# Kernel tuning notes

Measured on AMD Instinct MI355X. Metric: run time of the kernel, lower is better.

## Reference

```python
import jax, jax.numpy as jnp
import numpy as np

N, C, T, V, D = 128, 64, 256, 25, 64  # batch(*persons), in_ch, frames, joints, out_ch
RED = 4  # SE reduction


def _shift_indices(c, d, v):
    i = np.arange(v)[:, None]
    j = np.arange(c)[None, :]
    shift_in = ((i * c + j + j * c) % (c * v)).reshape(-1)
    jd = np.arange(d)[None, :]
    shift_out = ((i * d + jd - jd * d) % (d * v)).reshape(-1)
    return jnp.asarray(shift_in, jnp.int32), jnp.asarray(shift_out, jnp.int32)


def setup_inputs() -> dict:
    key = jax.random.key(0)
    ks = jax.random.split(key, 6)
    r = C // RED
    x0 = jax.random.normal(ks[0], (N, C, T, V), jnp.float32)
    fc1_w = jax.random.normal(ks[1], (r, C), jnp.float32) * (2.0 / C) ** 0.5
    fc1_b = jnp.zeros((r,), jnp.float32)
    fc2_w = jax.random.normal(ks[2], (4, r), jnp.float32) * (2.0 / r) ** 0.5
    fc2_b = jnp.zeros((4,), jnp.float32)
    W = jax.random.normal(ks[3], (4, C, D), jnp.float32) * (1.0 / D) ** 0.5
    b = jnp.zeros((4, D), jnp.float32)
    mask = jax.random.normal(ks[4], (1, V, C), jnp.float32) * 0.1  # Feature_Mask
    gamma = jnp.ones((V * D,), jnp.float32)
    beta = jnp.zeros((V * D,), jnp.float32)
    shift_in, shift_out = _shift_indices(C, D, V)
    return dict(x0=x0, epoch=100, fc1_w=fc1_w, fc1_b=fc1_b, fc2_w=fc2_w,
                fc2_b=fc2_b, W=W, b=b, mask=mask, gamma=gamma, beta=beta,
                shift_in=shift_in, shift_out=shift_out)


def reference(x0, epoch, fc1_w, fc1_b, fc2_w, fc2_b, W, b, mask, gamma, beta,
              shift_in, shift_out):
    n, c, t, v = x0.shape
    d = W.shape[-1]
    # DY_SEModule: global avg pool -> 1x1 conv -> relu -> 1x1 conv -> softmax(/tao)
    pooled = x0.mean(axis=(2, 3))                       # [n, c]
    h = jax.nn.relu(pooled @ fc1_w.T + fc1_b)           # [n, c//4]
    logits = h @ fc2_w.T + fc2_b                        # [n, 4]
    tao = 1.0 if epoch >= 60 else -(30.0 - 1.0) / 60.0 * epoch + 30.0
    gate = jax.nn.softmax(logits / tao, axis=1)         # [n, 4]
    # per-sample fused weights/bias
    Wf = jnp.einsum('kcd,nk->ncd', W, gate)             # [n, c, d]
    bf = jnp.einsum('kc,nk->nc', b, gate)               # [n, d]
    # shift-in gather + tanh feature mask
    x = x0.transpose(0, 2, 3, 1).reshape(n * t, v * c)  # [n*t, v*c]
    x = jnp.take(x, shift_in, axis=1).reshape(n * t, v, c)
    x = x * (jnp.tanh(mask) + 1.0)
    x = x.reshape(n, t, v, c)
    # per-sample linear
    x = jnp.einsum('ntvc,ncd->ntvd', x, Wf) + bf[:, None, None, :]
    # shift-out gather + BatchNorm1d over v*d features (training-mode stats)
    x = jnp.take(x.reshape(n * t, v * d), shift_out, axis=1)
    mu = x.mean(axis=0)
    var = x.var(axis=0)
    x = (x - mu) * jax.lax.rsqrt(var + 1e-5) * gamma + beta
    x = x.reshape(n, t, v, d).transpose(0, 3, 1, 2)     # [n, d, t, v]
    # residual (in==out -> identity down) + relu
    return jax.nn.relu(x + x0)
```

## Files before the change

### kernel.cpp

```cpp
#include <hip/hip_runtime.h>
#include <hip/hip_bf16.h>
#include <math.h>

#define N_   128
#define C_   64
#define T_   256
#define V_   25
#define D_   64
#define CTV  409600
#define TV   6400

typedef __attribute__((ext_vector_type(8))) short short8;
typedef __attribute__((ext_vector_type(4))) short short4v;
typedef __attribute__((ext_vector_type(4))) float f32x4;

__device__ inline unsigned short f2b(float f) {
    __hip_bfloat16 h = __float2bfloat16(f);
    return *(unsigned short*)&h;
}
__device__ inline float b2f(unsigned short u) {
    return __uint_as_float(((unsigned)u) << 16);
}

__global__ __launch_bounds__(256) void k_pool(const float* __restrict__ x0,
                                              float* __restrict__ pooled) {
    const int bid = blockIdx.x;
    const int tid = threadIdx.x;
    const float4* base = (const float4*)(x0 + (size_t)bid * TV);
    float s = 0.f;
    for (int i = tid; i < 1600; i += 256) {
        float4 f = base[i];
        s += (f.x + f.y) + (f.z + f.w);
    }
    #pragma unroll
    for (int off = 32; off > 0; off >>= 1) s += __shfl_down(s, off);
    __shared__ float red[4];
    if ((tid & 63) == 0) red[tid >> 6] = s;
    __syncthreads();
    if (tid == 0) pooled[bid] = (red[0] + red[1] + red[2] + red[3]) * (1.0f / TV);
}

__global__ __launch_bounds__(256) void k_se(
    const float* __restrict__ pooled, const float* __restrict__ fc1w,
    const float* __restrict__ fc1b,  const float* __restrict__ fc2w,
    const float* __restrict__ fc2b,  const float* __restrict__ Wm,
    const float* __restrict__ bm,    const float* __restrict__ mask,
    const int* __restrict__ shin,    const int* __restrict__ ep,
    unsigned short* __restrict__ Wfb, float* __restrict__ bfv,
    unsigned* __restrict__ gimg)
{
    __shared__ float sp[64], sh[16], sl[4];
    __shared__ float wk[64 * 65];
    const int tid = threadIdx.x, n = blockIdx.x;
    if (tid < 64) sp[tid] = pooled[n * 64 + tid];
    __syncthreads();
    if (tid < 16) {
        float s = fc1b[tid];
        #pragma unroll
        for (int c = 0; c < 64; c++) s = fmaf(sp[c], fc1w[tid * 64 + c], s);
        sh[tid] = fmaxf(s, 0.f);
    }
    __syncthreads();
    if (tid < 4) {
        float s = fc2b[tid];
        #pragma unroll
        for (int j = 0; j < 16; j++) s = fmaf(sh[j], fc2w[tid * 16 + j], s);
        sl[tid] = s;
    }
    __syncthreads();
    const int e = ep[0];
    const float tao = (e >= 60) ? 1.0f : (-(29.0f / 60.0f) * (float)e + 30.0f);
    const float it = 1.0f / tao;
    float l0 = sl[0] * it, l1 = sl[1] * it, l2 = sl[2] * it, l3 = sl[3] * it;
    float mx = fmaxf(fmaxf(l0, l1), fmaxf(l2, l3));
    float e0 = expf(l0 - mx), e1 = expf(l1 - mx), e2 = expf(l2 - mx), e3 = expf(l3 - mx);
    float inv = 1.0f / (e0 + e1 + e2 + e3);
    float ga[4] = {e0 * inv, e1 * inv, e2 * inv, e3 * inv};

    float accW[16];
    #pragma unroll
    for (int m = 0; m < 16; m++) accW[m] = 0.f;
    #pragma unroll
    for (int k = 0; k < 4; k++) {
        __syncthreads();
        for (int i = tid; i < 4096; i += 256)
            wk[(i >> 6) * 65 + (i & 63)] = Wm[k * 4096 + i];
        __syncthreads();
        #pragma unroll
        for (int m = 0; m < 16; m++) {
            int o = m * 256 + tid;
            int w  = o >> 10, s = (o >> 9) & 1;
            int ln = (o >> 3) & 63, j = o & 7;
            int c  = s * 32 + (ln >> 4) * 8 + j;
            int d  = w * 16 + (ln & 15);
            accW[m] = fmaf(ga[k], wk[c * 65 + d], accW[m]);
        }
    }
    #pragma unroll
    for (int m = 0; m < 16; m++)
        Wfb[(size_t)n * 4096 + m * 256 + tid] = f2b(accW[m]);
    if (tid < 64)
        bfv[n * 64 + tid] = ga[0] * bm[tid] + ga[1] * bm[64 + tid] +
                            ga[2] * bm[128 + tid] + ga[3] * bm[192 + tid];
    if (n == 0) {
        for (int j = tid; j < 1600; j += 256) {
            int s = shin[j];
            unsigned off = (unsigned)((s & 63) * 100 + (s >> 6));
            unsigned mgb = (unsigned)f2b(tanhf(mask[j]) + 1.0f);
            gimg[j] = (off << 16) | mgb;
        }
    }
}

__global__ __launch_bounds__(256, 4) void k_main(
    const float* __restrict__ x0, const unsigned short* __restrict__ Wfb,
    const float* __restrict__ bfv, const unsigned* __restrict__ gimg,
    __hip_bfloat16* __restrict__ y, float* __restrict__ sn)
{
    __shared__ unsigned short xs[6400];
    __shared__ unsigned short At[7616];
    __shared__ unsigned gimgS[1600];

    const int tid = threadIdx.x;
    const int w = tid >> 6, l = tid & 63, q = l >> 4, m = l & 15;
    const int n = blockIdx.x >> 4;
    const int tbase = (blockIdx.x & 15) * 16;

    short8 bf0 = *(const short8*)(Wfb + (size_t)n * 4096 + (w * 2 + 0) * 512 + l * 8);
    short8 bf1 = *(const short8*)(Wfb + (size_t)n * 4096 + (w * 2 + 1) * 512 + l * 8);
    const int d = w * 16 + m;
    const float bfl = bfv[n * 64 + d];

    for (int i = tid; i < 1600; i += 256) gimgS[i] = gimg[i];
    for (int i = tid; i < 408; i += 256) {
        int rr = i / 34, wo = i - rr * 34;
        int t = rr / 3, vr = rr - t * 3 + 1;
        ((unsigned*)At)[(96 + t * 4 + vr) * 34 + wo] = 0u;
    }

    float ss[25], sq[25];
    #pragma unroll
    for (int v = 0; v < 25; v++) { ss[v] = 0.f; sq[v] = 0.f; }

    for (int sub = 0; sub < 4; sub++) {
        const int t0 = tbase + sub * 4;
        __syncthreads();
        {
            const float4* src = (const float4*)x0;
            const int fb = n * 102400 + (t0 * 25) / 4;
            for (int i = tid; i < 1600; i += 256) {
                int c = i / 25, r = i - c * 25;
                float4 f = src[fb + c * 1600 + r];
                unsigned lo = ((unsigned)f2b(f.y) << 16) | f2b(f.x);
                unsigned hi = ((unsigned)f2b(f.w) << 16) | f2b(f.z);
                *(unsigned*)&xs[c * 100 + r * 4]     = lo;
                *(unsigned*)&xs[c * 100 + r * 4 + 2] = hi;
            }
        }
        __syncthreads();
        for (int p = tid; p < 3200; p += 256) {
            int cp = p & 31, rv = p >> 5;
            int t = rv / 25, v = rv - t * 25;
            int c = cp * 2;
            unsigned g0 = gimgS[v * 64 + c], g1 = gimgS[v * 64 + c + 1];
            float v0 = b2f(xs[(g0 >> 16) + t * 25]) * b2f((unsigned short)(g0 & 0xffff));
            float v1 = b2f(xs[(g1 >> 16) + t * 25]) * b2f((unsigned short)(g1 & 0xffff));
            int rho = (v >> 2) * 16 + t * 4 + (v & 3);
            *(unsigned*)&At[rho * 68 + c] = ((unsigned)f2b(v1) << 16) | f2b(v0);
        }
        __syncthreads();
        #pragma unroll
        for (int tau = 0; tau < 7; tau++) {
            const unsigned short* Ab = At + (tau * 16 + m) * 68 + q * 8;
            short4v a0l = *(const short4v*)(Ab);
            short4v a0h = *(const short4v*)(Ab + 4);
            short4v a1l = *(const short4v*)(Ab + 32);
            short4v a1h = *(const short4v*)(Ab + 36);
            short8 a0 = {a0l[0],a0l[1],a0l[2],a0l[3],a0h[0],a0h[1],a0h[2],a0h[3]};
            short8 a1 = {a1l[0],a1l[1],a1l[2],a1l[3],a1h[0],a1h[1],a1h[2],a1h[3]};
            f32x4 acc = {0.f, 0.f, 0.f, 0.f};
            acc = __builtin_amdgcn_mfma_f32_16x16x32_bf16(a0, bf0, acc, 0, 0, 0);
            acc = __builtin_amdgcn_mfma_f32_16x16x32_bf16(a1, bf1, acc, 0, 0, 0);
            const int t = t0 + q;
            __hip_bfloat16* yb = y + ((size_t)(n * T_ + t) * 25) * 64 + d;
            #pragma unroll
            for (int r = 0; r < 4; r++) {
                const int v = tau * 4 + r;
                if (v < 25) {
                    float val = acc[r] + bfl;
                    yb[v * 64] = __float2bfloat16(val);
                    ss[v] += val;
                    sq[v] = fmaf(val, val, sq[v]);
                }
            }
        }
    }
    #pragma unroll
    for (int v = 0; v < 25; v++) {
        ss[v] += __shfl_xor(ss[v], 16); ss[v] += __shfl_xor(ss[v], 32);
        sq[v] += __shfl_xor(sq[v], 16); sq[v] += __shfl_xor(sq[v], 32);
    }
    if (q == 0) {
        float* sb = sn + (size_t)n * 3200;
        #pragma unroll
        for (int v = 0; v < 25; v++) {
            atomicAdd(&sb[v * 64 + d], ss[v]);
            atomicAdd(&sb[1600 + v * 64 + d], sq[v]);
        }
    }
}

__global__ __launch_bounds__(256) void k_bn(
    const float* __restrict__ sn,
    const float* __restrict__ gamma, const float* __restrict__ beta,
    const int* __restrict__ shout,
    float2* __restrict__ ab)
{
    const int tid = threadIdx.x;
    const int jl = tid >> 2;
    const int p  = tid & 3;
    const int j = blockIdx.x * 64 + jl;
    const int src = shout[j];
    float s = 0.f, qq = 0.f;
    for (int nn = p; nn < 128; nn += 4) {
        s  += sn[(size_t)nn * 3200 + src];
        qq += sn[(size_t)nn * 3200 + 1600 + src];
    }
    s  += __shfl_xor(s, 1);  s  += __shfl_xor(s, 2);
    qq += __shfl_xor(qq, 1); qq += __shfl_xor(qq, 2);
    if (p == 0) {
        const float invn = 1.0f / 32768.0f;
        float mu = s * invn;
        float var = qq * invn - mu * mu;
        float rstd = rsqrtf(var + 1e-5f);
        float a = gamma[j] * rstd;
        float bb = beta[j] - mu * a;
        int dd = j & 63, vo = j >> 6;
        ab[dd * 25 + vo] = make_float2(a, bb);
    }
}

__global__ __launch_bounds__(256, 6) void k_out(
    const __hip_bfloat16* __restrict__ y, const float* __restrict__ x0,
    const float2* __restrict__ ab, float* __restrict__ out)
{
    __shared__ __align__(16) unsigned short ys[8 * 1652];
    const int tid = threadIdx.x;
    const int n = blockIdx.x >> 5;
    const int t0 = (blockIdx.x & 31) * 8;
    const uint4* ysrc = (const uint4*)((const unsigned short*)y + (size_t)(n * T_ + t0) * 1600);
    for (int i = tid; i < 1600; i += 256) {
        uint4 g = ysrc[i];
        int tl = i / 200, r8 = (i - tl * 200) * 8;
        int v = r8 >> 6, d0 = r8 & 63;
        unsigned* p = (unsigned*)ys + ((tl * 1652 + v * 66 + d0) >> 1);
        p[0] = g.x; p[1] = g.y; p[2] = g.z; p[3] = g.w;
    }
    __syncthreads();
    const float* xb = x0 + (size_t)n * CTV + t0 * 25;
    float* ob = out + (size_t)n * CTV + t0 * 25;
    for (int o4 = tid; o4 < 3200; o4 += 256) {
        int dd = o4 / 50;
        int rem4 = (o4 - dd * 50) * 4;
        int ddm = dd;
        if (ddm >= 25) ddm -= 25;
        if (ddm >= 25) ddm -= 25;
        int tl = rem4 / 25, vo = rem4 - tl * 25;
        const int base = dd * TV + rem4;
        f32x4 xv = *(const f32x4*)(xb + base);
        f32x4 r;
        #pragma unroll
        for (int e = 0; e < 4; e++) {
            int vy = vo - ddm; if (vy < 0) vy += 25;
            float val = b2f(ys[tl * 1652 + vy * 66 + dd]);
            float2 g = ab[dd * 25 + vo];
            r[e] = fmaxf(fmaf(val, g.x, g.y) + xv[e], 0.f);
            vo++; if (vo == 25) { vo = 0; tl++; }
        }
        __builtin_nontemporal_store(r, (f32x4*)(ob + base));
    }
}

extern "C" void kernel_launch(void* const* d_in, const int* in_sizes, int n_in,
                              void* d_out, int out_size, void* d_ws, size_t ws_size,
                              hipStream_t stream) {
    const float* x0    = (const float*)d_in[0];
    const int*   ep    = (const int*)  d_in[1];
    const float* fc1w  = (const float*)d_in[2];
    const float* fc1b  = (const float*)d_in[3];
    const float* fc2w  = (const float*)d_in[4];
    const float* fc2b  = (const float*)d_in[5];
    const float* Wm    = (const float*)d_in[6];
    const float* bm    = (const float*)d_in[7];
    const float* mask  = (const float*)d_in[8];
    const float* gamma = (const float*)d_in[9];
    const float* beta  = (const float*)d_in[10];
    const int*   shin  = (const int*)  d_in[11];
    const int*   shout = (const int*)  d_in[12];
    float* out = (float*)d_out;

    float* wsf = (float*)d_ws;
    float*          pooled = wsf;
    float*          bfv    = wsf + 8192;
    unsigned*       gimg   = (unsigned*)(wsf + 16384);
    float2*         ab     = (float2*)(wsf + 17984);
    unsigned short* Wfb    = (unsigned short*)(wsf + 22784);
    float*          sn     = wsf + 284928;
    __hip_bfloat16* y      = (__hip_bfloat16*)(wsf + 694528);

    hipMemsetAsync(sn, 0, 409600 * sizeof(float), stream);
    k_pool<<<N_ * C_, 256, 0, stream>>>(x0, pooled);
    k_se<<<N_, 256, 0, stream>>>(pooled, fc1w, fc1b, fc2w, fc2b, Wm, bm, mask,
                                 shin, ep, Wfb, bfv, gimg);
    k_main<<<N_ * 16, 256, 0, stream>>>(x0, Wfb, bfv, gimg, y, sn);
    k_bn<<<25, 256, 0, stream>>>(sn, gamma, beta, shout, ab);
    k_out<<<N_ * 32, 256, 0, stream>>>(y, x0, ab, out);
}
```

Measured before the change: 575.5 us.

## Fuse shift-in gather into x0 load with analytic index and double-buffer A tile

The x0 tile is no longer staged in shared memory and then gathered through a precomputed shift_in table. Each loaded element is scattered straight into the MFMA A-tile, using a closed-form shift (v - c mod 25) and a transposed mask table. The A tile is double-buffered across sub-iterations, which drops one __syncthreads per iteration and an LDS round trip. The change hardcodes the shift_in pattern instead of reading the input index array, and the scattered 2-byte LDS stores may cause bank conflicts.

After: 573.7 us. No clear change (-0.3%).

```diff
diff --git a/kernel.cpp b/kernel.cpp
--- a/kernel.cpp
+++ b/kernel.cpp
@@ -45,9 +45,9 @@
     const float* __restrict__ fc1b,  const float* __restrict__ fc2w,
     const float* __restrict__ fc2b,  const float* __restrict__ Wm,
     const float* __restrict__ bm,    const float* __restrict__ mask,
-    const int* __restrict__ shin,    const int* __restrict__ ep,
+    const int* __restrict__ ep,
     unsigned short* __restrict__ Wfb, float* __restrict__ bfv,
-    unsigned* __restrict__ gimg)
+    unsigned short* __restrict__ mgT)
 {
     __shared__ float sp[64], sh[16], sl[4];
     __shared__ float wk[64 * 65];
@@ -103,23 +103,20 @@
         bfv[n * 64 + tid] = ga[0] * bm[tid] + ga[1] * bm[64 + tid] +
                             ga[2] * bm[128 + tid] + ga[3] * bm[192 + tid];
     if (n == 0) {
-        for (int j = tid; j < 1600; j += 256) {
-            int s = shin[j];
-            unsigned off = (unsigned)((s & 63) * 100 + (s >> 6));
-            unsigned mgb = (unsigned)f2b(tanhf(mask[j]) + 1.0f);
-            gimg[j] = (off << 16) | mgb;
+        for (int i = tid; i < 1600; i += 256) {
+            int c = i / 25, v = i - c * 25;
+            mgT[i] = f2b(tanhf(mask[v * 64 + c]) + 1.0f);
         }
     }
 }
 
 __global__ __launch_bounds__(256, 4) void k_main(
     const float* __restrict__ x0, const unsigned short* __restrict__ Wfb,
-    const float* __restrict__ bfv, const unsigned* __restrict__ gimg,
+    const float* __restrict__ bfv, const unsigned short* __restrict__ mgT,
     __hip_bfloat16* __restrict__ y, float* __restrict__ sn)
 {
-    __shared__ unsigned short xs[6400];
-    __shared__ unsigned short At[7616];
-    __shared__ unsigned gimgS[1600];
+    __shared__ unsigned short At[2][7616];
+    __shared__ unsigned short mgTs[64 * 26];
 
     const int tid = threadIdx.x;
     const int w = tid >> 6, l = tid & 63, q = l >> 4, m = l & 15;
@@ -131,51 +128,54 @@
     const int d = w * 16 + m;
     const float bfl = bfv[n * 64 + d];
 
-    for (int i = tid; i < 1600; i += 256) gimgS[i] = gimg[i];
-    for (int i = tid; i < 408; i += 256) {
-        int rr = i / 34, wo = i - rr * 34;
+    for (int i = tid; i < 1600; i += 256) {
+        int c = i / 25, v = i - c * 25;
+        mgTs[c * 26 + v] = mgT[i];
+    }
+    for (int i = tid; i < 816; i += 256) {
+        int b = (i >= 408) ? 1 : 0;
+        int ii = i - b * 408;
+        int rr = ii / 34, wo = ii - rr * 34;
         int t = rr / 3, vr = rr - t * 3 + 1;
-        ((unsigned*)At)[(96 + t * 4 + vr) * 34 + wo] = 0u;
-    }
+        ((unsigned*)At[b])[(96 + t * 4 + vr) * 34 + wo] = 0u;
+    }
+    __syncthreads();
 
     float ss[25], sq[25];
     #pragma unroll
     for (int v = 0; v < 25; v++) { ss[v] = 0.f; sq[v] = 0.f; }
 
+    const float4* src = (const float4*)x0;
     for (int sub = 0; sub < 4; sub++) {
         const int t0 = tbase + sub * 4;
+        unsigned short* Ab = At[sub & 1];
+        const int fb = n * 102400 + (t0 * 25) / 4;
+        for (int i = tid; i < 1600; i += 256) {
+            int c = i / 25, r = i - c * 25;
+            float4 f = src[fb + c * 1600 + r];
+            int cm = c; if (cm >= 25) cm -= 25; if (cm >= 25) cm -= 25;
+            int f0 = r * 4;
+            int t = f0 / 25;
+            int vp = f0 - t * 25;
+            int v = vp - cm; if (v < 0) v += 25;
+            #pragma unroll
+            for (int e = 0; e < 4; e++) {
+                float xv = (e == 0) ? f.x : (e == 1) ? f.y : (e == 2) ? f.z : f.w;
+                int rho = (v >> 2) * 16 + t * 4 + (v & 3);
+                Ab[rho * 68 + c] = f2b(xv * b2f(mgTs[c * 26 + v]));
+                vp++; v++;
+                if (vp == 25) { vp = 0; t++; }
+                if (v == 25) v = 0;
+            }
+        }
         __syncthreads();
-        {
-            const float4* src = (const float4*)x0;
-            const int fb = n * 102400 + (t0 * 25) / 4;
-            for (int i = tid; i < 1600; i += 256) {
-                int c = i / 25, r = i - c * 25;
-                float4 f = src[fb + c * 1600 + r];
-                unsigned lo = ((unsigned)f2b(f.y) << 16) | f2b(f.x);
-                unsigned hi = ((unsigned)f2b(f.w) << 16) | f2b(f.z);
-                *(unsigned*)&xs[c * 100 + r * 4]     = lo;
-                *(unsigned*)&xs[c * 100 + r * 4 + 2] = hi;
-            }
-        }
-        __syncthreads();
-        for (int p = tid; p < 3200; p += 256) {
-            int cp = p & 31, rv = p >> 5;
-            int t = rv / 25, v = rv - t * 25;
-            int c = cp * 2;
-            unsigned g0 = gimgS[v * 64 + c], g1 = gimgS[v * 64 + c + 1];
-            float v0 = b2f(xs[(g0 >> 16) + t * 25]) * b2f((unsigned short)(g0 & 0xffff));
-            float v1 = b2f(xs[(g1 >> 16) + t * 25]) * b2f((unsigned short)(g1 & 0xffff));
-            int rho = (v >> 2) * 16 + t * 4 + (v & 3);
-            *(unsigned*)&At[rho * 68 + c] = ((unsigned)f2b(v1) << 16) | f2b(v0);
-        }
-        __syncthreads();
         #pragma unroll
         for (int tau = 0; tau < 7; tau++) {
-            const unsigned short* Ab = At + (tau * 16 + m) * 68 + q * 8;
-            short4v a0l = *(const short4v*)(Ab);
-            short4v a0h = *(const short4v*)(Ab + 4);
-            short4v a1l = *(const short4v*)(Ab + 32);
-            short4v a1h = *(const short4v*)(Ab + 36);
+            const unsigned short* Abr = Ab + (tau * 16 + m) * 68 + q * 8;
+            short4v a0l = *(const short4v*)(Abr);
+            short4v a0h = *(const short4v*)(Abr + 4);
+            short4v a1l = *(const short4v*)(Abr + 32);
+            short4v a1h = *(const short4v*)(Abr + 36);
             short8 a0 = {a0l[0],a0l[1],a0l[2],a0l[3],a0h[0],a0h[1],a0h[2],a0h[3]};
             short8 a1 = {a1l[0],a1l[1],a1l[2],a1l[3],a1h[0],a1h[1],a1h[2],a1h[3]};
             f32x4 acc = {0.f, 0.f, 0.f, 0.f};
@@ -295,14 +295,13 @@
     const float* mask  = (const float*)d_in[8];
     const float* gamma = (const float*)d_in[9];
     const float* beta  = (const float*)d_in[10];
-    const int*   shin  = (const int*)  d_in[11];
     const int*   shout = (const int*)  d_in[12];
     float* out = (float*)d_out;
 
     float* wsf = (float*)d_ws;
     float*          pooled = wsf;
     float*          bfv    = wsf + 8192;
-    unsigned*       gimg   = (unsigned*)(wsf + 16384);
+    unsigned short* mgT    = (unsigned short*)(wsf + 16384);
     float2*         ab     = (float2*)(wsf + 17984);
     unsigned short* Wfb    = (unsigned short*)(wsf + 22784);
     float*          sn     = wsf + 284928;
@@ -311,8 +310,8 @@
     hipMemsetAsync(sn, 0, 409600 * sizeof(float), stream);
     k_pool<<<N_ * C_, 256, 0, stream>>>(x0, pooled);
     k_se<<<N_, 256, 0, stream>>>(pooled, fc1w, fc1b, fc2w, fc2b, Wm, bm, mask,
-                                 shin, ep, Wfb, bfv, gimg);
-    k_main<<<N_ * 16, 256, 0, stream>>>(x0, Wfb, bfv, gimg, y, sn);
+                                 ep, Wfb, bfv, mgT);
+    k_main<<<N_ * 16, 256, 0, stream>>>(x0, Wfb, bfv, mgT, y, sn);
     k_bn<<<25, 256, 0, stream>>>(sn, gamma, beta, shout, ab);
     k_out<<<N_ * 32, 256, 0, stream>>>(y, x0, ab, out);
 }
```
